# Optimization experiments

Hardware: AMD Instinct MI355X
Metric: run time of the kernel (lower is better)

Reference implementation:

```python
import jax, jax.numpy as jnp
import numpy as np

# SSD-style extra-layer channel pyramid for sample_duration=16 (reconstructed):
CH = [(2048, 512, 1024), (1024, 256, 512), (512, 128, 256)]
DN = ('NCDHW', 'OIDHW', 'NCDHW')
B = 128


def conv3d(x, w, stride=(1, 1, 1), padding='VALID', rhs_dilation=None):
    return jax.lax.conv_general_dilated(
        x, w, window_strides=stride, padding=padding,
        rhs_dilation=rhs_dilation, dimension_numbers=DN)


def setup_inputs() -> dict:
    key = jax.random.key(0)
    ks = iter(jax.random.split(key, 32))
    s = 0.02
    d = {}
    d['x'] = jax.random.normal(next(ks), (B, 2048, 16, 2, 2), jnp.float32)
    d['start_boundaries'] = jax.random.randint(next(ks), (B,), 0, 1000, dtype=jnp.int32)
    # head 0 operates on the backbone feature map directly, kernel (2,2,2)
    d['loc_w0'] = s * jax.random.normal(next(ks), (2, 2048, 2, 2, 2), jnp.float32)
    d['conf_w0'] = s * jax.random.normal(next(ks), (3, 2048, 2, 2, 2), jnp.float32)
    for i, (cin, mid, cout) in enumerate(CH):
        d[f'e{i}_w1'] = s * jax.random.normal(next(ks), (mid, cin, 1, 1, 1), jnp.float32)
        d[f'e{i}_w2'] = s * jax.random.normal(next(ks), (cout, mid, 3, 3, 3), jnp.float32)
        d[f'loc_w{i+1}'] = s * jax.random.normal(next(ks), (2, cout, 2, 2, 2), jnp.float32)
        d[f'conf_w{i+1}'] = s * jax.random.normal(next(ks), (3, cout, 2, 2, 2), jnp.float32)
    return d


def reference(x, start_boundaries, loc_w0, conf_w0,
              e0_w1, e0_w2, loc_w1, conf_w1,
              e1_w1, e1_w2, loc_w2, conf_w2,
              e2_w1, e2_w2, loc_w3, conf_w3):
    del start_boundaries  # only used in test phase
    b = x.shape[0]
    loc_ws = [loc_w0, loc_w1, loc_w2, loc_w3]
    conf_ws = [conf_w0, conf_w1, conf_w2, conf_w3]
    extra = [(e0_w1, e0_w2), (e1_w1, e1_w2), (e2_w1, e2_w2)]
    locs = [conv3d(x, loc_ws[0]).reshape(b, -1)]
    confs = [conv3d(x, conf_ws[0]).reshape(b, -1)]
    h = x
    for i, (w1, w2) in enumerate(extra):
        h = conv3d(h, w1)  # 1x1x1 channel reduce
        # 3x3x3, temporal dilation/stride/padding 2 -> T halves, H/W preserved
        h = conv3d(h, w2, stride=(2, 1, 1),
                   padding=[(2, 2), (1, 1), (1, 1)], rhs_dilation=(2, 1, 1))
        locs.append(conv3d(h, loc_ws[i + 1]).reshape(b, -1))
        confs.append(conv3d(h, conf_ws[i + 1]).reshape(b, -1))
    loc = jnp.concatenate(locs, axis=1).reshape(b, -1, 2)    # [B, 26, 2]
    conf = jnp.concatenate(confs, axis=1).reshape(b, -1, 3)  # [B, 26, 3]
    return (loc, conf)
```

## Files before the change

### kernel.cpp

```cpp
#include <hip/hip_runtime.h>

typedef __bf16 bf16;
typedef bf16 bf16x2 __attribute__((ext_vector_type(2)));
typedef bf16 bf16x8 __attribute__((ext_vector_type(8)));
typedef float f32x4 __attribute__((ext_vector_type(4)));

__device__ __forceinline__ void gload16(const bf16* g, bf16* l) {
  __builtin_amdgcn_global_load_lds((const __attribute__((address_space(1))) void*)g,
                                   (__attribute__((address_space(3))) void*)l, 16, 0, 0);
}

template <bool FULL>
__global__ __launch_bounds__(256) void pack_x(const float* __restrict__ x, bf16* __restrict__ dstbuf) {
  __shared__ float tile[64 * 65];
  const int b = blockIdx.x, cb = blockIdx.y;
  const int t = threadIdx.x;
  const float* src = x + ((size_t)b * 2048 + cb * 64) * 64;
  #pragma unroll
  for (int p = 0; p < 16; ++p) {
    int idx = t + p * 256;
    tile[(idx >> 6) * 65 + (idx & 63)] = src[idx];
  }
  __syncthreads();
  if constexpr (FULL) {
    bf16* dst = dstbuf + (size_t)b * 131072 + cb * 64;
    #pragma unroll
    for (int p = 0; p < 8; ++p) {
      int idx = t + p * 256;
      int dhw = idx >> 5;
      int cl2 = (idx & 31) * 2;
      bf16x2 v;
      v.x = (bf16)tile[cl2 * 65 + dhw];
      v.y = (bf16)tile[(cl2 + 1) * 65 + dhw];
      *(bf16x2*)(dst + (size_t)dhw * 2048 + cl2) = v;
    }
  } else {
    bf16* dst = dstbuf + ((size_t)b * 32) * 2048 + cb * 64;
    const int cl2 = (t & 31) * 2, mr0 = t >> 5;
    #pragma unroll
    for (int p = 0; p < 4; ++p) {
      int mrow = mr0 + p * 8;
      int dd = mrow >> 2, hw = mrow & 3;
      int sdhw = dd * 8 + hw;
      bf16x2 v;
      v.x = (bf16)tile[cl2 * 65 + sdhw];
      v.y = (bf16)tile[(cl2 + 1) * 65 + sdhw];
      *(bf16x2*)(dst + (size_t)mrow * 2048 + cl2) = v;
    }
  }
}

__global__ __launch_bounds__(256) void pack_w0(const float* __restrict__ lw0,
                                               const float* __restrict__ cw0,
                                               bf16* __restrict__ Bh) {
  int idx = blockIdx.x * 256 + threadIdx.x;
  int n = idx >> 13, k = idx & 8191;
  int hw = k >> 11, c = k & 2047;
  float v = 0.f;
  if (n < 10) {
    int kd = n / 5, j = n % 5;
    const float* w = (j < 2) ? (lw0 + j * 16384) : (cw0 + (j - 2) * 16384);
    v = w[c * 8 + kd * 4 + hw];
  }
  Bh[idx] = (bf16)v;
}

__global__ __launch_bounds__(256) void head0_gemm(const bf16* __restrict__ xcl,
                                                  const bf16* __restrict__ Bh,
                                                  float* __restrict__ P) {
  __shared__ bf16 ldsA[64 * 64];
  __shared__ bf16 ldsB[16 * 64];
  const int bm = blockIdx.x, ks = blockIdx.y;
  const int tid = threadIdx.x;
  const int wv = tid >> 6, lane = tid & 63, r = lane & 15, g = lane >> 4;
  f32x4 acc = {0.f, 0.f, 0.f, 0.f};
  for (int k0 = 0; k0 < 1024; k0 += 64) {
    #pragma unroll
    for (int q = 0; q < 2; ++q) {
      int idx = tid + q * 256;
      int row = idx >> 3, cg = idx & 7;
      gload16(xcl + (size_t)(bm * 64 + row) * 8192 + ks * 1024 + k0 + (cg ^ (row & 7)) * 8,
              ldsA + idx * 8);
    }
    if (tid < 128) {
      int row = tid >> 3, cg = tid & 7;
      gload16(Bh + (size_t)row * 8192 + ks * 1024 + k0 + (cg ^ (row & 7)) * 8,
              ldsB + tid * 8);
    }
    __syncthreads();
    #pragma unroll
    for (int ks2 = 0; ks2 < 2; ++ks2) {
      int rowa = wv * 16 + r;
      bf16x8 af = *(const bf16x8*)(ldsA + rowa * 64 + ((ks2 * 4 + g) ^ (rowa & 7)) * 8);
      bf16x8 bf_ = *(const bf16x8*)(ldsB + r * 64 + ((ks2 * 4 + g) ^ (r & 7)) * 8);
      acc = __builtin_amdgcn_mfma_f32_16x16x32_bf16(af, bf_, acc, 0, 0, 0);
    }
    __syncthreads();
  }
  const int m = bm * 64 + wv * 16 + g * 4;
  #pragma unroll
  for (int jr = 0; jr < 4; ++jr)
    P[(size_t)(ks * 2048 + m + jr) * 16 + r] = acc[jr];
}

__global__ __launch_bounds__(128) void head0_combine(const float* __restrict__ P,
                                                     float* __restrict__ out) {
  const int b = blockIdx.x, t = threadIdx.x;
  if (t < 75) {
    int j = t / 15, d = t % 15;
    float s = 0.f;
    #pragma unroll
    for (int ks = 0; ks < 8; ++ks) {
      const float* pb = P + (size_t)(ks * 2048 + b * 16) * 16;
      s += pb[d * 16 + j] + pb[(d + 1) * 16 + 5 + j];
    }
    if (j < 2) out[b * 52 + j * 15 + d] = s;
    else       out[6656 + b * 78 + (j - 2) * 15 + d] = s;
  }
}

__global__ __launch_bounds__(256) void cvt_w1(const float* __restrict__ in, bf16* __restrict__ out, int n8) {
  int i = blockIdx.x * 256 + threadIdx.x;
  if (i < n8) {
    const float4* p = (const float4*)(in + (size_t)i * 8);
    float4 a = p[0], b = p[1];
    bf16x8 v = {(bf16)a.x, (bf16)a.y, (bf16)a.z, (bf16)a.w,
                (bf16)b.x, (bf16)b.y, (bf16)b.z, (bf16)b.w};
    *(bf16x8*)(out + (size_t)i * 8) = v;
  }
}

__global__ __launch_bounds__(256) void pack_w2(const float* __restrict__ w2, bf16* __restrict__ w2p,
                                               int oBase, int cin) {
  __shared__ float tile[64 * 27];
  const int orel = blockIdx.x, cb = blockIdx.y;
  const int o = oBase + orel;
  const float* src = w2 + ((size_t)o * cin + cb * 64) * 27;
  const int t = threadIdx.x;
  for (int idx = t; idx < 1728; idx += 256) tile[idx] = src[idx];
  __syncthreads();
  bf16* dst = w2p + (size_t)orel * 27 * cin + cb * 64;
  for (int idx = t; idx < 1728; idx += 256) {
    int tap = idx >> 6, cl = idx & 63;
    dst[(size_t)tap * cin + cl] = (bf16)tile[cl * 27 + tap];
  }
}

struct GP {
  const bf16* A; const bf16* B; bf16* O;
  int K;
  int ashb, asB, am1, as1, am2, as2;
  int oshb, osB, om1, os1, om2, os2, oOff;
  int lgCv, coutS, oCol0, lgCin;
};

template <int FM, int FN, bool W2M>
__global__ __launch_bounds__(256) void gemm_bf(GP p) {
  constexpr int BM = FM * 32, BN = FN * 32;
  __shared__ bf16 lds[(BM + BN) * 64];
  bf16* ldsA = lds;
  bf16* ldsB = lds + BM * 64;
  const int tid = threadIdx.x;
  const int bm = blockIdx.x, bn = blockIdx.y;

  int aBase[BM / 32], aL[BM / 32];
  #pragma unroll
  for (int q = 0; q < BM / 32; ++q) {
    int idx = tid + q * 256;
    int row = idx >> 3, cg = idx & 7;
    int m = bm * BM + row;
    aBase[q] = (m >> p.ashb) * p.asB + ((m >> 2) & p.am1) * p.as1 + (m & p.am2) * p.as2;
    aL[q] = ((cg ^ row) & 7) * 8;
  }
  int opk[BN / 32];
  int bN[BN / 32], bL[BN / 32];
  int khkw0 = 0, khkw1 = 0, khkw2 = 0, khkw3 = 0;
  #pragma unroll
  for (int q = 0; q < BN / 32; ++q) {
    int idx = tid + q * 256;
    int row = idx >> 3, cg = idx & 7;
    int n = bn * BN + row;
    int sw = ((cg ^ row) & 7) * 8;
    if constexpr (W2M) {
      int op = n & ((1 << p.lgCv) - 1);
      opk[q] = (op * 27 << p.lgCin) + sw;
      bN[q] = 0; bL[q] = 0;
    } else {
      bN[q] = n; bL[q] = sw; opk[q] = 0;
    }
  }
  if constexpr (W2M) {
    const int hwp = (bn * BN) >> p.lgCv;
    const int hp = hwp >> 1, wp = hwp & 1;
    khkw0 = ((1 - hp) * 3 + (1 - wp)) << p.lgCin;
    khkw1 = ((1 - hp) * 3 + (2 - wp)) << p.lgCin;
    khkw2 = ((2 - hp) * 3 + (1 - wp)) << p.lgCin;
    khkw3 = ((2 - hp) * 3 + (2 - wp)) << p.lgCin;
  }

  const int wv = tid >> 6, wm = wv >> 1, wn = wv & 1;
  const int lane = tid & 63, r = lane & 15, g = lane >> 4;

  f32x4 acc[FM][FN];
  const f32x4 zz = {0.f, 0.f, 0.f, 0.f};
  #pragma unroll
  for (int i = 0; i < FM; ++i)
    #pragma unroll
    for (int j = 0; j < FN; ++j) acc[i][j] = zz;

  for (int k0 = 0; k0 < p.K; k0 += 64) {
    #pragma unroll
    for (int q = 0; q < BM / 32; ++q) {
      int idx = tid + q * 256;
      gload16(p.A + aBase[q] + k0 + aL[q], ldsA + idx * 8);
    }
    if constexpr (W2M) {
      const int kd = k0 >> (p.lgCin + 2);
      const int hwsel = (k0 >> p.lgCin) & 3;
      const int c0 = k0 & ((1 << p.lgCin) - 1);
      int kk = (hwsel & 2) ? ((hwsel & 1) ? khkw3 : khkw2)
                           : ((hwsel & 1) ? khkw1 : khkw0);
      const int koff = (kd * 9 << p.lgCin) + kk + c0;
      #pragma unroll
      for (int q = 0; q < BN / 32; ++q) {
        int idx = tid + q * 256;
        gload16(p.B + opk[q] + koff, ldsB + idx * 8);
      }
    } else {
      #pragma unroll
      for (int q = 0; q < BN / 32; ++q) {
        int idx = tid + q * 256;
        gload16(p.B + (size_t)bN[q] * p.K + k0 + bL[q], ldsB + idx * 8);
      }
    }
    __syncthreads();
    #pragma unroll
    for (int ks = 0; ks < 2; ++ks) {
      bf16x8 af[FM], bfr[FN];
      #pragma unroll
      for (int i = 0; i < FM; ++i) {
        int row = wm * FM * 16 + i * 16 + r;
        int pcg = (ks * 4 + g) ^ (row & 7);
        af[i] = *(const bf16x8*)(ldsA + row * 64 + pcg * 8);
      }
      #pragma unroll
      for (int j = 0; j < FN; ++j) {
        int row = wn * FN * 16 + j * 16 + r;
        int pcg = (ks * 4 + g) ^ (row & 7);
        bfr[j] = *(const bf16x8*)(ldsB + row * 64 + pcg * 8);
      }
      #pragma unroll
      for (int i = 0; i < FM; ++i)
        #pragma unroll
        for (int j = 0; j < FN; ++j)
          acc[i][j] = __builtin_amdgcn_mfma_f32_16x16x32_bf16(af[i], bfr[j], acc[i][j], 0, 0, 0);
    }
    __syncthreads();
  }

  #pragma unroll
  for (int i = 0; i < FM; ++i) {
    #pragma unroll
    for (int j = 0; j < FN; ++j) {
      int ncol = bn * BN + wn * FN * 16 + j * 16 + r;
      int outcol = (ncol >> p.lgCv) * p.coutS + p.oCol0 + (ncol & ((1 << p.lgCv) - 1));
      #pragma unroll
      for (int jr = 0; jr < 4; ++jr) {
        int m = bm * BM + wm * FM * 16 + i * 16 + g * 4 + jr;
        int oa = (m >> p.oshb) * p.osB + ((m >> 2) & p.om1) * p.os1 + (m & p.om2) * p.os2 + p.oOff + outcol;
        p.O[oa] = (bf16)acc[i][j][jr];
      }
    }
  }
}

__global__ __launch_bounds__(256) void gemm2_db(const bf16* __restrict__ A,
                                                const bf16* __restrict__ B,
                                                bf16* __restrict__ O) {
  __shared__ bf16 lds[2][16384];
  const int tid = threadIdx.x;
  const int bm = blockIdx.x, bn = blockIdx.y;

  int aOff[4], bOff[4];
  #pragma unroll
  for (int q = 0; q < 4; ++q) {
    int idx = tid + q * 256;
    int row = idx >> 3, cg = idx & 7;
    int sw = ((cg ^ row) & 7) * 8;
    int m = bm * 128 + row;
    aOff[q] = (m >> 3) * 20480 + (m & 7) * 2048 + sw;
    int n = bn * 128 + row;
    bOff[q] = (n & 1023) * 13824 + sw;
  }
  const int hwp = (bn * 128) >> 10;
  const int hp = hwp >> 1, wp = hwp & 1;
  const int kk0 = ((1 - hp) * 3 + (1 - wp)) << 9;
  const int kk1 = ((1 - hp) * 3 + (2 - wp)) << 9;
  const int kk2 = ((2 - hp) * 3 + (1 - wp)) << 9;
  const int kk3 = ((2 - hp) * 3 + (2 - wp)) << 9;

  const int wv = tid >> 6, wm = wv >> 1, wn = wv & 1;
  const int lane = tid & 63, r = lane & 15, g = lane >> 4;

  f32x4 acc[4][4];
  const f32x4 zz = {0.f, 0.f, 0.f, 0.f};
  #pragma unroll
  for (int i = 0; i < 4; ++i)
    #pragma unroll
    for (int j = 0; j < 4; ++j) acc[i][j] = zz;

  auto koffOf = [&](int k0) {
    int kd = k0 >> 11, hws = (k0 >> 9) & 3, c0 = k0 & 511;
    int kk = (hws & 2) ? ((hws & 1) ? kk3 : kk2) : ((hws & 1) ? kk1 : kk0);
    return kd * 4608 + kk + c0;
  };

  {
    int ko = koffOf(0);
    #pragma unroll
    for (int q = 0; q < 4; ++q) {
      int idx = tid + q * 256;
      gload16(A + aOff[q], &lds[0][idx * 8]);
      gload16(B + bOff[q] + ko, &lds[0][8192 + idx * 8]);
    }
  }
  __syncthreads();

  int cur = 0;
  for (int t = 0; t < 96; ++t) {
    if (t < 95) {
      int k1 = (t + 1) * 64;
      int ko = koffOf(k1);
      int nb = cur ^ 1;
      #pragma unroll
      for (int q = 0; q < 4; ++q) {
        int idx = tid + q * 256;
        gload16(A + aOff[q] + k1, &lds[nb][idx * 8]);
        gload16(B + bOff[q] + ko, &lds[nb][8192 + idx * 8]);
      }
    }
    __builtin_amdgcn_sched_barrier(0);
    const bf16* LA = lds[cur];
    const bf16* LB = lds[cur] + 8192;
    #pragma unroll
    for (int ks = 0; ks < 2; ++ks) {
      bf16x8 af[4], bfr[4];
      #pragma unroll
      for (int i = 0; i < 4; ++i) {
        int row = wm * 64 + i * 16 + r;
        int pcg = (ks * 4 + g) ^ (row & 7);
        af[i] = *(const bf16x8*)(LA + row * 64 + pcg * 8);
      }
      #pragma unroll
      for (int j = 0; j < 4; ++j) {
        int row = wn * 64 + j * 16 + r;
        int pcg = (ks * 4 + g) ^ (row & 7);
        bfr[j] = *(const bf16x8*)(LB + row * 64 + pcg * 8);
      }
      #pragma unroll
      for (int i = 0; i < 4; ++i)
        #pragma unroll
        for (int j = 0; j < 4; ++j)
          acc[i][j] = __builtin_amdgcn_mfma_f32_16x16x32_bf16(af[i], bfr[j], acc[i][j], 0, 0, 0);
    }
    __syncthreads();
    cur ^= 1;
  }

  #pragma unroll
  for (int i = 0; i < 4; ++i) {
    #pragma unroll
    for (int j = 0; j < 4; ++j) {
      int n = bn * 128 + wn * 64 + j * 16 + r;
      #pragma unroll
      for (int jr = 0; jr < 4; ++jr) {
        int m = bm * 128 + wm * 64 + i * 16 + g * 4 + jr;
        O[(size_t)m * 4096 + n] = (bf16)acc[i][j][jr];
      }
    }
  }
}

template <typename T, bool XL>
__global__ __launch_bounds__(256)
void heads_k(const T* __restrict__ in, const float* __restrict__ wl,
             const float* __restrict__ wc, float* __restrict__ out,
             const int C, const int dcnt, const int sB, const int sD,
             const int sHW, const int sC, const int loff, const int coff) {
  const int tid = threadIdx.x;
  const int blk = blockIdx.x;
  const int b = blk / dcnt, d = blk - b * dcnt;
  float a0 = 0, a1 = 0, c0 = 0, c1 = 0, c2 = 0;
  const int C8 = C * 8;
  if constexpr (XL) {
    const int hw = tid & 3, kd = (tid >> 2) & 1, cb = tid >> 3;
    const int base = b * sB + (d + kd) * sD + hw * sHW;
    const int wb = kd * 4 + hw;
    for (int i = 0; i < C / 32; ++i) {
      const int c = cb + i * 32;
      const float v = (float)in[base + c * sC];
      const int wi = c * 8 + wb;
      a0 += v * wl[wi];  a1 += v * wl[C8 + wi];
      c0 += v * wc[wi];  c1 += v * wc[C8 + wi];  c2 += v * wc[2 * C8 + wi];
    }
  } else {
    for (int c = tid; c < C; c += 256) {
      #pragma unroll
      for (int kd = 0; kd < 2; ++kd) {
        #pragma unroll
        for (int hw = 0; hw < 4; ++hw) {
          const float v = (float)in[b * sB + (d + kd) * sD + hw * sHW + c];
          const int wi = c * 8 + kd * 4 + hw;
          a0 += v * wl[wi];  a1 += v * wl[C8 + wi];
          c0 += v * wc[wi];  c1 += v * wc[C8 + wi];  c2 += v * wc[2 * C8 + wi];
        }
      }
    }
  }
  #pragma unroll
  for (int off = 32; off; off >>= 1) {
    a0 += __shfl_down(a0, off, 64);
    a1 += __shfl_down(a1, off, 64);
    c0 += __shfl_down(c0, off, 64);
    c1 += __shfl_down(c1, off, 64);
    c2 += __shfl_down(c2, off, 64);
  }
  __shared__ float red[5][4];
  const int lane = tid & 63, wv = tid >> 6;
  if (lane == 0) { red[0][wv] = a0; red[1][wv] = a1; red[2][wv] = c0; red[3][wv] = c1; red[4][wv] = c2; }
  __syncthreads();
  if (tid == 0) {
    float L0 = red[0][0] + red[0][1] + red[0][2] + red[0][3];
    float L1 = red[1][0] + red[1][1] + red[1][2] + red[1][3];
    float F0 = red[2][0] + red[2][1] + red[2][2] + red[2][3];
    float F1 = red[3][0] + red[3][1] + red[3][2] + red[3][3];
    float F2 = red[4][0] + red[4][1] + red[4][2] + red[4][3];
    float* loc = out + (size_t)b * 52 + loff;
    loc[0 * dcnt + d] = L0;
    loc[1 * dcnt + d] = L1;
    float* cf = out + 6656 + (size_t)b * 78 + coff;
    cf[0 * dcnt + d] = F0;
    cf[1 * dcnt + d] = F1;
    cf[2 * dcnt + d] = F2;
  }
}

extern "C" void kernel_launch(void* const* d_in, const int* in_sizes, int n_in,
                              void* d_out, int out_size, void* d_ws, size_t ws_size,
                              hipStream_t stream) {
  (void)in_sizes; (void)n_in; (void)out_size;
  const float* x    = (const float*)d_in[0];
  const float* lw0  = (const float*)d_in[2];
  const float* cw0  = (const float*)d_in[3];
  const float* e0w1 = (const float*)d_in[4];
  const float* e0w2 = (const float*)d_in[5];
  const float* lw1  = (const float*)d_in[6];
  const float* cw1  = (const float*)d_in[7];
  const float* e1w1 = (const float*)d_in[8];
  const float* e1w2 = (const float*)d_in[9];
  const float* lw2  = (const float*)d_in[10];
  const float* cw2  = (const float*)d_in[11];
  const float* e2w1 = (const float*)d_in[12];
  const float* e2w2 = (const float*)d_in[13];
  const float* lw3  = (const float*)d_in[14];
  const float* cw3  = (const float*)d_in[15];
  float* out = (float*)d_out;
  bf16* W = (bf16*)d_ws;

  if (ws_size >= (size_t)49283072) {
    const size_t xclo = 0;
    const size_t W1f  = 16777216;
    const size_t h1af = 17825792;
    const size_t h1bf = 20447232;
    const size_t w2p0f = 0;
    const size_t W1c1f = 0, h2af = 262144, w2p1f = 1048576, h2bf = 4587520;
    const size_t W1c2f = 6684672, h3af = 6750208, w2p2f = 7012352, h3bf = 7897088;
    bf16* Bh = W + h1bf;
    float* P = (float*)(W + h1bf + 131072);

    hipMemsetAsync(W + h1af, 0, (size_t)2621440 * 2, stream);
    pack_x<true><<<dim3(128, 32), 256, 0, stream>>>(x, W + xclo);
    pack_w0<<<512, 256, 0, stream>>>(lw0, cw0, Bh);
    head0_gemm<<<dim3(32, 8), 256, 0, stream>>>(W + xclo, Bh, P);
    head0_combine<<<128, 128, 0, stream>>>(P, out);
    cvt_w1<<<512, 256, 0, stream>>>(e0w1, W + W1f, 131072);

    GP g1 = {W + xclo, W + W1f, W + h1af, 2048,
             5, 131072, 7, 16384, 3, 2048,
             5, 20480, 7, 2048, 3, 512, 2048,
             9, 512, 0, 0};
    gemm_bf<2, 2, false><<<dim3(64, 8), 256, 0, stream>>>(g1);

    pack_w2<<<dim3(1024, 8), 256, 0, stream>>>(e0w2, W + w2p0f, 0, 512);
    gemm2_db<<<dim3(8, 32), 256, 0, stream>>>(W + h1af, W + w2p0f, W + h1bf);
    heads_k<bf16, false><<<128 * 7, 256, 0, stream>>>(
        W + h1bf, lw1, cw1, out, 1024, 7, 32768, 4096, 1024, 1, 30, 45);

    hipMemsetAsync(W + h2af, 0, (size_t)786432 * 2, stream);
    cvt_w1<<<128, 256, 0, stream>>>(e1w1, W + W1c1f, 32768);
    GP g3 = {W + h1bf, W + W1c1f, W + h2af, 1024,
             4, 32768, 3, 8192, 3, 1024,
             4, 6144, 3, 1024, 3, 256, 1024,
             8, 256, 0, 0};
    gemm_bf<1, 1, false><<<dim3(64, 8), 256, 0, stream>>>(g3);
    pack_w2<<<dim3(512, 4), 256, 0, stream>>>(e1w2, W + w2p1f, 0, 256);
    GP g4 = {W + h2af, W + w2p1f, W + h2bf, 3072,
             2, 6144, 0, 0, 3, 1024,
             0, 2048, 0, 0, 0, 0, 0,
             9, 512, 0, 8};
    gemm_bf<1, 1, true><<<dim3(16, 64), 256, 0, stream>>>(g4);
    heads_k<bf16, false><<<128 * 3, 256, 0, stream>>>(
        W + h2bf, lw2, cw2, out, 512, 3, 8192, 2048, 512, 1, 44, 66);

    hipMemsetAsync(W + h3af, 0, (size_t)262144 * 2, stream);
    cvt_w1<<<32, 256, 0, stream>>>(e2w1, W + W1c2f, 8192);
    GP g5 = {W + h2bf, W + W1c2f, W + h3af, 512,
             3, 8192, 1, 4096, 3, 512,
             3, 2048, 1, 512, 3, 128, 512,
             7, 128, 0, 0};
    gemm_bf<1, 1, false><<<dim3(32, 4), 256, 0, stream>>>(g5);
    pack_w2<<<dim3(256, 2), 256, 0, stream>>>(e2w2, W + w2p2f, 0, 128);
    GP g6 = {W + h3af, W + w2p2f, W + h3bf, 1536,
             1, 2048, 0, 0, 1, 512,
             0, 1024, 0, 0, 0, 0, 0,
             8, 256, 0, 7};
    gemm_bf<1, 1, true><<<dim3(8, 32), 256, 0, stream>>>(g6);
    heads_k<bf16, false><<<128 * 1, 256, 0, stream>>>(
        W + h3bf, lw3, cw3, out, 256, 1, 2048, 1024, 256, 1, 50, 75);
    return;
  }

  const size_t A0o  = 0;
  const size_t W1o  = 8388608;
  const size_t h1ao = 9437184;
  const size_t h1bo = 12058624;
  const size_t W1c1 = 8388608, W1c2 = 8650752, h3ao = 8716288, h3bo = 8978432;
  const size_t h2ao = 9437184, h2bo = 12058624;
  const size_t w2p0o = 0, w2p1o = 0, w2p2o = 3538944;

  hipMemsetAsync(W + h1ao, 0, (size_t)2621440 * 2, stream);
  pack_x<false><<<dim3(128, 32), 256, 0, stream>>>(x, W + A0o);
  cvt_w1<<<512, 256, 0, stream>>>(e0w1, W + W1o, 131072);

  GP g1 = {W + A0o, W + W1o, W + h1ao, 2048,
           0, 2048, 0, 0, 0, 0,
           5, 20480, 7, 2048, 3, 512, 2048,
           9, 512, 0, 0};
  gemm_bf<2, 2, false><<<dim3(64, 8), 256, 0, stream>>>(g1);

  pack_w2<<<dim3(512, 8), 256, 0, stream>>>(e0w2, W + w2p0o, 0, 512);
  GP g2a = {W + h1ao, W + w2p0o, W + h1bo, 6144,
            3, 20480, 0, 0, 7, 2048,
            0, 4096, 0, 0, 0, 0, 0,
            9, 1024, 0, 9};
  gemm_bf<2, 2, true><<<dim3(16, 32), 256, 0, stream>>>(g2a);
  pack_w2<<<dim3(512, 8), 256, 0, stream>>>(e0w2, W + w2p0o, 512, 512);
  GP g2b = {W + h1ao, W + w2p0o, W + h1bo, 6144,
            3, 20480, 0, 0, 7, 2048,
            0, 4096, 0, 0, 0, 0, 0,
            9, 1024, 512, 9};
  gemm_bf<2, 2, true><<<dim3(16, 32), 256, 0, stream>>>(g2b);

  heads_k<bf16, false><<<128 * 7, 256, 0, stream>>>(
      W + h1bo, lw1, cw1, out, 1024, 7, 32768, 4096, 1024, 1, 30, 45);

  hipMemsetAsync(W + h2ao, 0, (size_t)786432 * 2, stream);
  cvt_w1<<<128, 256, 0, stream>>>(e1w1, W + W1c1, 32768);
  GP g3 = {W + h1bo, W + W1c1, W + h2ao, 1024,
           4, 32768, 3, 8192, 3, 1024,
           4, 6144, 3, 1024, 3, 256, 1024,
           8, 256, 0, 0};
  gemm_bf<1, 1, false><<<dim3(64, 8), 256, 0, stream>>>(g3);
  pack_w2<<<dim3(512, 4), 256, 0, stream>>>(e1w2, W + w2p1o, 0, 256);
  GP g4 = {W + h2ao, W + w2p1o, W + h2bo, 3072,
           2, 6144, 0, 0, 3, 1024,
           0, 2048, 0, 0, 0, 0, 0,
           9, 512, 0, 8};
  gemm_bf<1, 1, true><<<dim3(16, 64), 256, 0, stream>>>(g4);
  heads_k<bf16, false><<<128 * 3, 256, 0, stream>>>(
      W + h2bo, lw2, cw2, out, 512, 3, 8192, 2048, 512, 1, 44, 66);

  hipMemsetAsync(W + h3ao, 0, (size_t)262144 * 2, stream);
  cvt_w1<<<32, 256, 0, stream>>>(e2w1, W + W1c2, 8192);
  GP g5 = {W + h2bo, W + W1c2, W + h3ao, 512,
           3, 8192, 1, 4096, 3, 512,
           3, 2048, 1, 512, 3, 128, 512,
           7, 128, 0, 0};
  gemm_bf<1, 1, false><<<dim3(32, 4), 256, 0, stream>>>(g5);
  pack_w2<<<dim3(256, 2), 256, 0, stream>>>(e2w2, W + w2p2o, 0, 128);
  GP g6 = {W + h3ao, W + w2p2o, W + h3bo, 1536,
           1, 2048, 0, 0, 1, 512,
           0, 1024, 0, 0, 0, 0, 0,
           8, 256, 0, 7};
  gemm_bf<1, 1, true><<<dim3(8, 32), 256, 0, stream>>>(g6);
  heads_k<bf16, false><<<128 * 1, 256, 0, stream>>>(
      W + h3bo, lw3, cw3, out, 256, 1, 2048, 1024, 256, 1, 50, 75);

  heads_k<float, true><<<128 * 15, 256, 0, stream>>>(
      x, lw0, cw0, out, 2048, 15, 131072, 4, 1, 64, 0, 0);
}
```

Before: 283.2 us.

## Split-K the first 3x3x3 conv GEMM with fp32 atomic accumulation

Replaces the double-buffered gemm2_db with a split-K variant (two K halves via grid z) that accumulates into an fp32 workspace using atomic adds, followed by a conversion kernel to bf16. The goal is more blocks in flight than the 256-block grid, which underfills the GPU's CUs. In exchange it drops LDS double buffering, adds a 16MB memset, atomic traffic and an extra conversion pass. The older workspace path now uses the generic gemm_bf, and the tail layers are factored into a helper.

```diff
diff --git a/kernel.cpp b/kernel.cpp
--- a/kernel.cpp
+++ b/kernel.cpp
@@ -274,12 +274,14 @@
   }
 }
 
-__global__ __launch_bounds__(256) void gemm2_db(const bf16* __restrict__ A,
+__global__ __launch_bounds__(256) void gemm2_sk(const bf16* __restrict__ A,
                                                 const bf16* __restrict__ B,
-                                                bf16* __restrict__ O) {
-  __shared__ bf16 lds[2][16384];
+                                                float* __restrict__ Hf) {
+  __shared__ bf16 lds[16384];
+  bf16* ldsA = lds;
+  bf16* ldsB = lds + 8192;
   const int tid = threadIdx.x;
-  const int bm = blockIdx.x, bn = blockIdx.y;
+  const int bm = blockIdx.x, bn = blockIdx.y, z = blockIdx.z;
 
   int aOff[4], bOff[4];
   #pragma unroll
@@ -309,39 +311,18 @@
     #pragma unroll
     for (int j = 0; j < 4; ++j) acc[i][j] = zz;
 
-  auto koffOf = [&](int k0) {
+  const int kbeg = z * 3072, kend = kbeg + 3072;
+  for (int k0 = kbeg; k0 < kend; k0 += 64) {
     int kd = k0 >> 11, hws = (k0 >> 9) & 3, c0 = k0 & 511;
     int kk = (hws & 2) ? ((hws & 1) ? kk3 : kk2) : ((hws & 1) ? kk1 : kk0);
-    return kd * 4608 + kk + c0;
-  };
-
-  {
-    int ko = koffOf(0);
+    int koff = kd * 4608 + kk + c0;
     #pragma unroll
     for (int q = 0; q < 4; ++q) {
       int idx = tid + q * 256;
-      gload16(A + aOff[q], &lds[0][idx * 8]);
-      gload16(B + bOff[q] + ko, &lds[0][8192 + idx * 8]);
-    }
-  }
-  __syncthreads();
-
-  int cur = 0;
-  for (int t = 0; t < 96; ++t) {
-    if (t < 95) {
-      int k1 = (t + 1) * 64;
-      int ko = koffOf(k1);
-      int nb = cur ^ 1;
-      #pragma unroll
-      for (int q = 0; q < 4; ++q) {
-        int idx = tid + q * 256;
-        gload16(A + aOff[q] + k1, &lds[nb][idx * 8]);
-        gload16(B + bOff[q] + ko, &lds[nb][8192 + idx * 8]);
-      }
-    }
-    __builtin_amdgcn_sched_barrier(0);
-    const bf16* LA = lds[cur];
-    const bf16* LB = lds[cur] + 8192;
+      gload16(A + aOff[q] + k0, ldsA + idx * 8);
+      gload16(B + bOff[q] + koff, ldsB + idx * 8);
+    }
+    __syncthreads();
     #pragma unroll
     for (int ks = 0; ks < 2; ++ks) {
       bf16x8 af[4], bfr[4];
@@ -349,13 +330,13 @@
       for (int i = 0; i < 4; ++i) {
         int row = wm * 64 + i * 16 + r;
         int pcg = (ks * 4 + g) ^ (row & 7);
-        af[i] = *(const bf16x8*)(LA + row * 64 + pcg * 8);
+        af[i] = *(const bf16x8*)(ldsA + row * 64 + pcg * 8);
       }
       #pragma unroll
       for (int j = 0; j < 4; ++j) {
         int row = wn * 64 + j * 16 + r;
         int pcg = (ks * 4 + g) ^ (row & 7);
-        bfr[j] = *(const bf16x8*)(LB + row * 64 + pcg * 8);
+        bfr[j] = *(const bf16x8*)(ldsB + row * 64 + pcg * 8);
       }
       #pragma unroll
       for (int i = 0; i < 4; ++i)
@@ -364,21 +345,30 @@
           acc[i][j] = __builtin_amdgcn_mfma_f32_16x16x32_bf16(af[i], bfr[j], acc[i][j], 0, 0, 0);
     }
     __syncthreads();
-    cur ^= 1;
   }
 
   #pragma unroll
   for (int i = 0; i < 4; ++i) {
     #pragma unroll
     for (int j = 0; j < 4; ++j) {
-      int n = bn * 128 + wn * 64 + j * 16 + r;
+      int col = bn * 128 + wn * 64 + j * 16 + r;
       #pragma unroll
       for (int jr = 0; jr < 4; ++jr) {
-        int m = bm * 128 + wm * 64 + i * 16 + g * 4 + jr;
-        O[(size_t)m * 4096 + n] = (bf16)acc[i][j][jr];
-      }
-    }
-  }
+        int rw = bm * 128 + wm * 64 + i * 16 + g * 4 + jr;
+        unsafeAtomicAdd(&Hf[(size_t)rw * 4096 + col], acc[i][j][jr]);
+      }
+    }
+  }
+}
+
+__global__ __launch_bounds__(256) void cvt_h1b(const float* __restrict__ Hf,
+                                               bf16* __restrict__ h1b) {
+  size_t base = ((size_t)blockIdx.x * 256 + threadIdx.x) * 8;
+  const float4* p = (const float4*)(Hf + base);
+  float4 a = p[0], b = p[1];
+  bf16x8 v = {(bf16)a.x, (bf16)a.y, (bf16)a.z, (bf16)a.w,
+              (bf16)b.x, (bf16)b.y, (bf16)b.z, (bf16)b.w};
+  *(bf16x8*)(h1b + base) = v;
 }
 
 template <typename T, bool XL>
@@ -445,6 +435,50 @@
   }
 }
 
+static void tail_layers(bf16* W, bf16* h1b, float* out,
+                        const float* e1w1, const float* e1w2,
+                        const float* lw2p, const float* cw2p,
+                        const float* e2w1, const float* e2w2,
+                        const float* lw3, const float* cw3,
+                        const float* lw1, const float* cw1,
+                        size_t W1c1, size_t h2a, size_t w2p1, size_t h2b,
+                        size_t W1c2, size_t h3a, size_t w2p2, size_t h3b,
+                        hipStream_t stream) {
+  heads_k<bf16, false><<<128 * 7, 256, 0, stream>>>(
+      h1b, lw1, cw1, out, 1024, 7, 32768, 4096, 1024, 1, 30, 45);
+  hipMemsetAsync(W + h2a, 0, (size_t)786432 * 2, stream);
+  cvt_w1<<<128, 256, 0, stream>>>(e1w1, W + W1c1, 32768);
+  GP g3 = {h1b, W + W1c1, W + h2a, 1024,
+           4, 32768, 3, 8192, 3, 1024,
+           4, 6144, 3, 1024, 3, 256, 1024,
+           8, 256, 0, 0};
+  gemm_bf<1, 1, false><<<dim3(64, 8), 256, 0, stream>>>(g3);
+  pack_w2<<<dim3(512, 4), 256, 0, stream>>>(e1w2, W + w2p1, 0, 256);
+  GP g4 = {W + h2a, W + w2p1, W + h2b, 3072,
+           2, 6144, 0, 0, 3, 1024,
+           0, 2048, 0, 0, 0, 0, 0,
+           9, 512, 0, 8};
+  gemm_bf<1, 1, true><<<dim3(16, 64), 256, 0, stream>>>(g4);
+  heads_k<bf16, false><<<128 * 3, 256, 0, stream>>>(
+      W + h2b, lw2p, cw2p, out, 512, 3, 8192, 2048, 512, 1, 44, 66);
+
+  hipMemsetAsync(W + h3a, 0, (size_t)262144 * 2, stream);
+  cvt_w1<<<32, 256, 0, stream>>>(e2w1, W + W1c2, 8192);
+  GP g5 = {W + h2b, W + W1c2, W + h3a, 512,
+           3, 8192, 1, 4096, 3, 512,
+           3, 2048, 1, 512, 3, 128, 512,
+           7, 128, 0, 0};
+  gemm_bf<1, 1, false><<<dim3(32, 4), 256, 0, stream>>>(g5);
+  pack_w2<<<dim3(256, 2), 256, 0, stream>>>(e2w2, W + w2p2, 0, 128);
+  GP g6 = {W + h3a, W + w2p2, W + h3b, 1536,
+           1, 2048, 0, 0, 1, 512,
+           0, 1024, 0, 0, 0, 0, 0,
+           8, 256, 0, 7};
+  gemm_bf<1, 1, true><<<dim3(8, 32), 256, 0, stream>>>(g6);
+  heads_k<bf16, false><<<128 * 1, 256, 0, stream>>>(
+      W + h3b, lw3, cw3, out, 256, 1, 2048, 1024, 256, 1, 50, 75);
+}
+
 extern "C" void kernel_launch(void* const* d_in, const int* in_sizes, int n_in,
                               void* d_out, int out_size, void* d_ws, size_t ws_size,
                               hipStream_t stream) {
@@ -467,14 +501,45 @@
   float* out = (float*)d_out;
   bf16* W = (bf16*)d_ws;
 
+  if (ws_size >= (size_t)50400000) {
+    const size_t xclo = 0;
+    const size_t W1f  = 16777216;
+    const size_t Bho  = 17825792;
+    const size_t Po   = 17956864;
+    const size_t h1ao = 22544384;
+    const size_t w2p0 = 8388608;
+    float* Hf = (float*)W;
+    bf16* h1b = W + 8388608;
+
+    hipMemsetAsync(W + h1ao, 0, (size_t)2621440 * 2, stream);
+    pack_x<true><<<dim3(128, 32), 256, 0, stream>>>(x, W + xclo);
+    pack_w0<<<512, 256, 0, stream>>>(lw0, cw0, W + Bho);
+    head0_gemm<<<dim3(32, 8), 256, 0, stream>>>(W + xclo, W + Bho, (float*)(W + Po));
+    head0_combine<<<128, 128, 0, stream>>>((float*)(W + Po), out);
+    cvt_w1<<<512, 256, 0, stream>>>(e0w1, W + W1f, 131072);
+
+    GP g1 = {W + xclo, W + W1f, W + h1ao, 2048,
+             5, 131072, 7, 16384, 3, 2048,
+             5, 20480, 7, 2048, 3, 512, 2048,
+             9, 512, 0, 0};
+    gemm_bf<2, 2, false><<<dim3(64, 8), 256, 0, stream>>>(g1);
+
+    hipMemsetAsync(Hf, 0, (size_t)16777216, stream);
+    pack_w2<<<dim3(1024, 8), 256, 0, stream>>>(e0w2, W + w2p0, 0, 512);
+    gemm2_sk<<<dim3(8, 32, 2), 256, 0, stream>>>(W + h1ao, W + w2p0, Hf);
+    cvt_h1b<<<2048, 256, 0, stream>>>(Hf, h1b);
+
+    tail_layers(W, h1b, out, e1w1, e1w2, lw2, cw2, e2w1, e2w2, lw3, cw3, lw1, cw1,
+                0, 262144, 1048576, 4587520, 6684672, 6750208, 7012352, 7897088, stream);
+    return;
+  }
+
   if (ws_size >= (size_t)49283072) {
     const size_t xclo = 0;
     const size_t W1f  = 16777216;
     const size_t h1af = 17825792;
     const size_t h1bf = 20447232;
     const size_t w2p0f = 0;
-    const size_t W1c1f = 0, h2af = 262144, w2p1f = 1048576, h2bf = 4587520;
-    const size_t W1c2f = 6684672, h3af = 6750208, w2p2f = 7012352, h3bf = 7897088;
     bf16* Bh = W + h1bf;
     float* P = (float*)(W + h1bf + 131072);
 
@@ -492,41 +557,14 @@
     gemm_bf<2, 2, false><<<dim3(64, 8), 256, 0, stream>>>(g1);
 
     pack_w2<<<dim3(1024, 8), 256, 0, stream>>>(e0w2, W + w2p0f, 0, 512);
-    gemm2_db<<<dim3(8, 32), 256, 0, stream>>>(W + h1af, W + w2p0f, W + h1bf);
-    heads_k<bf16, false><<<128 * 7, 256, 0, stream>>>(
-        W + h1bf, lw1, cw1, out, 1024, 7, 32768, 4096, 1024, 1, 30, 45);
-
-    hipMemsetAsync(W + h2af, 0, (size_t)786432 * 2, stream);
-    cvt_w1<<<128, 256, 0, stream>>>(e1w1, W + W1c1f, 32768);
-    GP g3 = {W + h1bf, W + W1c1f, W + h2af, 1024,
-             4, 32768, 3, 8192, 3, 1024,
-             4, 6144, 3, 1024, 3, 256, 1024,
-             8, 256, 0, 0};
-    gemm_bf<1, 1, false><<<dim3(64, 8), 256, 0, stream>>>(g3);
-    pack_w2<<<dim3(512, 4), 256, 0, stream>>>(e1w2, W + w2p1f, 0, 256);
-    GP g4 = {W + h2af, W + w2p1f, W + h2bf, 3072,
-             2, 6144, 0, 0, 3, 1024,
-             0, 2048, 0, 0, 0, 0, 0,
-             9, 512, 0, 8};
-    gemm_bf<1, 1, true><<<dim3(16, 64), 256, 0, stream>>>(g4);
-    heads_k<bf16, false><<<128 * 3, 256, 0, stream>>>(
-        W + h2bf, lw2, cw2, out, 512, 3, 8192, 2048, 512, 1, 44, 66);
-
-    hipMemsetAsync(W + h3af, 0, (size_t)262144 * 2, stream);
-    cvt_w1<<<32, 256, 0, stream>>>(e2w1, W + W1c2f, 8192);
-    GP g5 = {W + h2bf, W + W1c2f, W + h3af, 512,
-             3, 8192, 1, 4096, 3, 512,
-             3, 2048, 1, 512, 3, 128, 512,
-             7, 128, 0, 0};
-    gemm_bf<1, 1, false><<<dim3(32, 4), 256, 0, stream>>>(g5);
-    pack_w2<<<dim3(256, 2), 256, 0, stream>>>(e2w2, W + w2p2f, 0, 128);
-    GP g6 = {W + h3af, W + w2p2f, W + h3bf, 1536,
-             1, 2048, 0, 0, 1, 512,
-             0, 1024, 0, 0, 0, 0, 0,
-             8, 256, 0, 7};
-    gemm_bf<1, 1, true><<<dim3(8, 32), 256, 0, stream>>>(g6);
-    heads_k<bf16, false><<<128 * 1, 256, 0, stream>>>(
-        W + h3bf, lw3, cw3, out, 256, 1, 2048, 1024, 256, 1, 50, 75);
+    GP g2 = {W + h1af, W + w2p0f, W + h1bf, 6144,
+             3, 20480, 0, 0, 7, 2048,
+             0, 4096, 0, 0, 0, 0, 0,
+             10, 1024, 0, 9};
+    gemm_bf<2, 2, true><<<dim3(16, 64), 256, 0, stream>>>(g2);
+
+    tail_layers(W, W + h1bf, out, e1w1, e1w2, lw2, cw2, e2w1, e2w2, lw3, cw3, lw1, cw1,
+                0, 262144, 1048576, 4587520, 6684672, 6750208, 7012352, 7897088, stream);
     return;
   }
 
```

Result: faster. 267.1 us (-5.7%).
